# Performance work log

Hardware: AMD Instinct MI355X
Metric: run time of the kernel (lower is better)

The kernel has to match this reference:

```python
import jax, jax.numpy as jnp
import numpy as np

NEG_BIG = 1e9  # large-negative bias used by the original TF code


def setup_inputs() -> dict:
    key = jax.random.key(0)
    kq, kk, kv = jax.random.split(key, 3)
    B, H, W, C, CV = 8, 64, 64, 128, 128
    return {
        "query": jax.random.normal(kq, (B, H, W, C), dtype=jnp.float32),
        "key": jax.random.normal(kk, (B, H, W, C), dtype=jnp.float32),
        "value": jax.random.normal(kv, (B, H, W, CV), dtype=jnp.float32),
    }


def reference(query, key, value):
    B, Hh, Ww, C = query.shape
    CV = value.shape[-1]
    Nq = Hh * Ww                      # canvas_size_q (flattened spatial)
    Nk = key.shape[1] * key.shape[2]  # canvas_size
    q = query.reshape(B, Nq, C)
    k = key.reshape(B, Nk, C)
    v = value.reshape(B, Nk, CV)
    # dense QK^T scores over the flattened canvas: [B, Nq, Nk]
    dot = jnp.einsum('bqc,bkc->bqk', q, k) / jnp.sqrt(jnp.asarray(C, dtype=q.dtype))
    # causal mask: 1 where key position j <= query position i (allowed)
    allowed = jnp.tril(jnp.ones((Nq, Nk), dtype=q.dtype))
    # softmax with large-negative bias on disallowed positions, then re-mask
    probs = jax.nn.softmax(dot - NEG_BIG * (1.0 - allowed), axis=-1) * allowed
    mixed = jnp.einsum('bqk,bkc->bqc', probs, v)
    return mixed.reshape(B, Hh, Ww, CV)
```

## Files before the change

kernel.cpp:

```cpp
#include <hip/hip_runtime.h>
#include <hip/hip_bf16.h>

typedef __bf16 bf16_t;
typedef __attribute__((ext_vector_type(8))) __bf16 bf16x8;
typedef __attribute__((ext_vector_type(4))) __bf16 bf16x4;
typedef __attribute__((ext_vector_type(4))) float floatx4;

static constexpr int NSEQ = 4096;
static constexpr int DIM  = 128;
static constexpr int BATCH = 8;
static constexpr size_t NELEM = (size_t)BATCH * NSEQ * DIM;
static constexpr size_t WS_NEED = 2 * NELEM * sizeof(bf16_t);

static constexpr int NSLOT = 160;
static constexpr size_t WS_SPLITK =
    WS_NEED + (size_t)BATCH * NSLOT * (8192 + 64) * sizeof(float);

static constexpr float SCALE_LOG2E = 0.08838834764831845f * 1.4426950408889634f;

__device__ __forceinline__ int slot_base(int qt) {
  int g = qt >> 4, r = qt & 15;
  return qt + 8 * g * (g - 1) + r * g;
}

__device__ __forceinline__ void gld16(bf16_t* l, const bf16_t* g) {
  __builtin_amdgcn_global_load_lds(
      (const __attribute__((address_space(1))) unsigned int*)g,
      (__attribute__((address_space(3))) unsigned int*)l, 16, 0, 0);
}

__device__ __forceinline__ bf16x8 ld8_f32s(const float* p, float s) {
  float4 a = *(const float4*)p;
  float4 b = *(const float4*)(p + 4);
  bf16x8 r = {(__bf16)(a.x * s), (__bf16)(a.y * s), (__bf16)(a.z * s), (__bf16)(a.w * s),
              (__bf16)(b.x * s), (__bf16)(b.y * s), (__bf16)(b.z * s), (__bf16)(b.w * s)};
  return r;
}


__global__ __launch_bounds__(256)
void prep_kernel(const float* __restrict__ K, const float* __restrict__ V,
                 bf16_t* __restrict__ Kb, bf16_t* __restrict__ Vt) {
  __shared__ bf16_t ldsT[128 * 66];
  const int bid = blockIdx.x;
  if (bid < 1536) {
    const size_t n4 = NELEM / 4;
    for (size_t i = (size_t)bid * 256 + threadIdx.x; i < n4; i += (size_t)1536 * 256) {
      float4 k = ((const float4*)K)[i];
      bf16x4 kv = {(__bf16)k.x, (__bf16)k.y, (__bf16)k.z, (__bf16)k.w};
      ((bf16x4*)Kb)[i] = kv;
    }
  } else {
    const int id = bid - 1536;
    const int b  = id & 7;
    const int kt = id >> 3;
    const float* src = V + ((size_t)(b * NSEQ + kt * 64)) * DIM;
    #pragma unroll
    for (int it = 0; it < 8; ++it) {
      const int idx = it * 256 + (int)threadIdx.x;
      const int k = idx >> 5, c4 = idx & 31;
      float4 v = ((const float4*)src)[idx];
      ldsT[(c4 * 4 + 0) * 66 + k] = (__bf16)v.x;
      ldsT[(c4 * 4 + 1) * 66 + k] = (__bf16)v.y;
      ldsT[(c4 * 4 + 2) * 66 + k] = (__bf16)v.z;
      ldsT[(c4 * 4 + 3) * 66 + k] = (__bf16)v.w;
    }
    __syncthreads();
    #pragma unroll
    for (int it = 0; it < 4; ++it) {
      const int task = it * 256 + (int)threadIdx.x;
      const int d = task >> 3, kg = task & 7;
      bf16x8 o;
      #pragma unroll
      for (int j = 0; j < 8; ++j) o[j] = ldsT[d * 66 + kg * 8 + j];
      *(bf16x8*)(Vt + ((size_t)b * DIM + d) * NSEQ + kt * 64 + kg * 8) = o;
    }
  }
}


template <bool MASK>
__device__ __forceinline__ void tile16(
    const bf16_t* __restrict__ kbuf, const bf16_t* __restrict__ vbuf,
    const bf16x8 (&qf)[4], int l16, int quad, int wq16,
    floatx4 (&acc)[8], float& lsum) {
  #pragma unroll
  for (int h = 0; h < 2; ++h) {
    float pr[8];
    #pragma unroll
    for (int cc = 0; cc < 2; ++cc) {
      const int c4 = 2 * h + cc;
      floatx4 sv = {0.f, 0.f, 0.f, 0.f};
      const bf16_t* krow = kbuf + (c4 * 16 + l16) * DIM;
      #pragma unroll
      for (int d = 0; d < 4; ++d) {
        bf16x8 kf = *(const bf16x8*)(krow + (((4 * d + quad) ^ l16) * 8));
        sv = __builtin_amdgcn_mfma_f32_16x16x32_bf16(kf, qf[d], sv, 0, 0, 0);
      }
      #pragma unroll
      for (int r = 0; r < 4; ++r) {
        float v = sv[r];
        if constexpr (MASK) {
          const int key = 32 * h + 8 * quad + 4 * cc + r;
          v = (key <= wq16 + l16) ? v : -3.0e38f;
        }
        float p = __builtin_amdgcn_exp2f(v);
        lsum += p;
        pr[4 * cc + r] = p;
      }
    }
    bf16x8 pf;
    #pragma unroll
    for (int j = 0; j < 8; ++j) pf[j] = (__bf16)pr[j];
    __builtin_amdgcn_s_setprio(1);
    #pragma unroll
    for (int c = 0; c < 8; ++c) {
      const bf16_t* vrow = vbuf + (c * 16 + l16) * 64;
      bf16x8 vf = *(const bf16x8*)(vrow + (((quad + 4 * h) ^ (l16 & 7)) * 8));
      acc[c] = __builtin_amdgcn_mfma_f32_16x16x32_bf16(pf, vf, acc[c], 0, 0, 0);
    }
    __builtin_amdgcn_s_setprio(0);
  }
}


__global__ __launch_bounds__(256, 3)
void causal_attn_splitk(const float* __restrict__ Qf, const bf16_t* __restrict__ Kb,
                        const bf16_t* __restrict__ Vt, float* __restrict__ Out,
                        float* __restrict__ Pp, float* __restrict__ Ls) {
  __shared__ __align__(16) bf16_t Kds[2][64 * DIM];
  __shared__ __align__(16) bf16_t Vds[DIM * 64];

  const int b = (int)blockIdx.x & 7;
  const int s = (NSLOT - 1) - ((int)blockIdx.x >> 3);
  int qt = 63, cch = 0;
  {
    int acc0 = 0;
    #pragma unroll
    for (int g = 0; g < 4; ++g) {
      const int bandw = 16 * (g + 1);
      if (s < acc0 + bandw) {
        const int u = s - acc0;
        qt = g * 16 + u / (g + 1);
        cch = u % (g + 1);
        break;
      }
      acc0 += bandw;
    }
  }
  const int ntot = qt + 1;
  const int nch  = (qt >> 4) + 1;
  const int nt_c = (ntot - 1 - cch) / nch + 1;
  const int nmask = (cch + (nt_c - 1) * nch == qt) ? 1 : 0;
  const int nfull = nt_c - nmask;

  const int tid  = (int)threadIdx.x;
  const int wave = tid >> 6;
  const int lane = tid & 63;
  const int l16  = lane & 15;
  const int quad = lane >> 4;
  const int wq16 = wave * 16;

  bf16x8 qf[4];
  {
    const float* qrow =
        Qf + ((size_t)b * NSEQ + qt * 64 + wq16 + l16) * DIM + quad * 8;
    #pragma unroll
    for (int d = 0; d < 4; ++d) qf[d] = ld8_f32s(qrow + 32 * d, SCALE_LOG2E);
  }

  const bf16_t* kg = Kb + (size_t)b * NSEQ * DIM;
  const bf16_t* vg = Vt + ((size_t)b * DIM + 32 * wave) * NSEQ;
  int koff[4], voff[4], vsrc[4], vdst[4];
  #pragma unroll
  for (int i = 0; i < 4; ++i) {
    const int p    = 16 * wave + 4 * i + quad;
    const int srow = 32 * (wave >> 1) + 8 * i + 4 * (wave & 1) + quad;
    koff[i] = srow * DIM + ((l16 ^ (p & 15)) * 8);
    const int vrow = 8 * i + (lane >> 3);
    voff[i] = vrow * NSEQ + (((lane & 7) ^ (vrow & 7)) * 8);
    vsrc[i] = vrow * NSEQ + (lane & 7) * 8;
    vdst[i] = (32 * wave + vrow) * 64 + (((lane & 7) ^ (vrow & 7)) * 8);
  }

  floatx4 acc[8];
  #pragma unroll
  for (int c = 0; c < 8; ++c) acc[c] = (floatx4){0.f, 0.f, 0.f, 0.f};
  float lsum = 0.f;

  {
    const size_t kb0 = (size_t)cch * 64;
    bf16_t* kl = &Kds[0][wave * 2048];
    bf16_t* vl = &Vds[wave * 2048];
    #pragma unroll
    for (int i = 0; i < 4; ++i) {
      gld16(kl + i * 512, kg + kb0 * DIM + koff[i]);
      gld16(vl + i * 512, vg + kb0 + voff[i]);
    }
  }
  __syncthreads();

  bf16x8 vreg[4];
  int t = cch;
  for (int it = 0; it < nt_c; ++it, t += nch) {
    const int cur = it & 1;
    const bool more = (it + 1 < nt_c);
    const size_t kbn = (size_t)(t + nch) * 64;
    if (more) {
      bf16_t* kl = &Kds[cur ^ 1][wave * 2048];
      #pragma unroll
      for (int i = 0; i < 4; ++i) gld16(kl + i * 512, kg + kbn * DIM + koff[i]);
      #pragma unroll
      for (int i = 0; i < 4; ++i) vreg[i] = *(const bf16x8*)(vg + kbn + vsrc[i]);
    }
    __builtin_amdgcn_sched_barrier(0);
    if (it < nfull)
      tile16<false>(Kds[cur], Vds, qf, l16, quad, wq16, acc, lsum);
    else
      tile16<true>(Kds[cur], Vds, qf, l16, quad, wq16, acc, lsum);
    __builtin_amdgcn_sched_barrier(0);
    __builtin_amdgcn_s_barrier();
    if (more) {
      #pragma unroll
      for (int i = 0; i < 4; ++i) *(bf16x8*)(&Vds[vdst[i]]) = vreg[i];
      asm volatile("s_waitcnt lgkmcnt(0)" ::: "memory");
      __builtin_amdgcn_sched_barrier(0);
      __builtin_amdgcn_s_barrier();
    }
  }

  float lred = lsum;
  lred += __shfl_xor(lred, 16, 64);
  lred += __shfl_xor(lred, 32, 64);

  if (nch == 1) {
    float invl[4];
    #pragma unroll
    for (int r = 0; r < 4; ++r)
      invl[r] = 1.0f / __shfl(lred, quad * 4 + r, 64);
    float* orow =
        Out + ((size_t)b * NSEQ + qt * 64 + wq16 + quad * 4) * DIM + l16;
    #pragma unroll
    for (int c = 0; c < 8; ++c)
      #pragma unroll
      for (int r = 0; r < 4; ++r)
        orow[(size_t)r * DIM + c * 16] = acc[c][r] * invl[r];
  } else {
    const int slot = b * NSLOT + slot_base(qt) + cch;
    float* pb = Pp + (size_t)slot * 8192 +
                ((size_t)(wq16 + quad * 4)) * 128 + l16;
    #pragma unroll
    for (int c = 0; c < 8; ++c)
      #pragma unroll
      for (int r = 0; r < 4; ++r)
        pb[(size_t)r * 128 + c * 16] = acc[c][r];
    if (quad == 0)
      Ls[(size_t)slot * 64 + wq16 + l16] = lred;
  }
}


__global__ __launch_bounds__(256)
void combine_kernel(const float* __restrict__ Pp, const float* __restrict__ Ls,
                    float* __restrict__ Out) {
  const int e    = (int)blockIdx.x >> 1;
  const int half = (int)blockIdx.x & 1;
  const int b    = e & 7;
  const int qt   = 16 + (e >> 3);
  const int s0   = b * NSLOT + slot_base(qt);
  const int nch  = (qt >> 4) + 1;
  const int t = (int)threadIdx.x;
  #pragma unroll
  for (int j = 0; j < 4; ++j) {
    const int idx = j * 256 + t;
    const int q   = half * 32 + (idx >> 5);
    const int d4  = idx & 31;
    float4 v = {0.f, 0.f, 0.f, 0.f};
    float  l = 0.f;
    for (int ch = 0; ch < nch; ++ch) {
      const float* pc = Pp + (size_t)(s0 + ch) * 8192 + (size_t)q * 128 + d4 * 4;
      float4 a = *(const float4*)pc;
      v.x += a.x; v.y += a.y; v.z += a.z; v.w += a.w;
      l += Ls[(size_t)(s0 + ch) * 64 + q];
    }
    const float inv = 1.0f / l;
    float4 r = {v.x * inv, v.y * inv, v.z * inv, v.w * inv};
    *(float4*)(Out + ((size_t)b * NSEQ + qt * 64 + q) * DIM + d4 * 4) = r;
  }
}


template <bool MASK>
__device__ __forceinline__ void tile_compute(
    const bf16_t* __restrict__ kbuf, const bf16_t* __restrict__ vbuf,
    bf16_t* __restrict__ pl, const bf16x8 (&qf)[4],
    int l16, int quad, int wq, floatx4 (&acc)[8], float (&lsum)[4]) {
  floatx4 s[4];
  #pragma unroll
  for (int c4 = 0; c4 < 4; ++c4) s[c4] = (floatx4){0.f, 0.f, 0.f, 0.f};
  #pragma unroll
  for (int c4 = 0; c4 < 4; ++c4) {
    const bf16_t* krow = kbuf + (c4 * 16 + l16) * DIM;
    #pragma unroll
    for (int d = 0; d < 4; ++d) {
      bf16x8 kf = *(const bf16x8*)(krow + (((4 * d + quad) ^ l16) * 8));
      s[c4] = __builtin_amdgcn_mfma_f32_16x16x32_bf16(qf[d], kf, s[c4], 0, 0, 0);
    }
  }
  #pragma unroll
  for (int c4 = 0; c4 < 4; ++c4) {
    #pragma unroll
    for (int r = 0; r < 4; ++r) {
      float v = s[c4][r];
      if constexpr (MASK)
        v = (c4 * 16 + l16 <= wq + quad * 4 + r) ? v : -3.0e38f;
      float p = __builtin_amdgcn_exp2f(v);
      lsum[r] += p;
      pl[(quad * 4 + r) * 72 + c4 * 16 + l16] = (__bf16)p;
    }
  }
  asm volatile("s_waitcnt lgkmcnt(0)" ::: "memory");
  bf16x8 pfA = *(const bf16x8*)(pl + l16 * 72 + quad * 8);
  bf16x8 pfB = *(const bf16x8*)(pl + l16 * 72 + 32 + quad * 8);
  #pragma unroll
  for (int c = 0; c < 8; ++c) {
    const bf16_t* vrow = vbuf + (c * 16 + l16) * 64;
    bf16x8 vfA = *(const bf16x8*)(vrow + ((quad ^ (l16 & 7)) * 8));
    bf16x8 vfB = *(const bf16x8*)(vrow + (((quad + 4) ^ (l16 & 7)) * 8));
    acc[c] = __builtin_amdgcn_mfma_f32_16x16x32_bf16(pfA, vfA, acc[c], 0, 0, 0);
    acc[c] = __builtin_amdgcn_mfma_f32_16x16x32_bf16(pfB, vfB, acc[c], 0, 0, 0);
  }
}

__global__ __launch_bounds__(256)
void causal_attn_kernel(const float* __restrict__ Qf, const bf16_t* __restrict__ Kb,
                        const bf16_t* __restrict__ Vt, float* __restrict__ Out) {
  __shared__ __align__(16) bf16_t Kbuf[64 * DIM];
  __shared__ __align__(16) bf16_t Vbuf[DIM * 64];
  __shared__ __align__(16) bf16_t Pbuf[4][16 * 72];

  const int half = blockIdx.x >> 8;
  const int idx  = blockIdx.x & 255;
  const int b    = idx & 7;
  const int q32  = idx >> 3;
  const int qt64 = half ? q32 : 63 - q32;

  const int tid  = (int)threadIdx.x;
  const int wave = tid >> 6;
  const int lane = tid & 63;
  const int l16  = lane & 15;
  const int quad = lane >> 4;
  const int wq   = wave * 16;

  bf16x8 qf[4];
  {
    const float* qrow = Qf + ((size_t)b * NSEQ + qt64 * 64 + wq + l16) * DIM + quad * 8;
    #pragma unroll
    for (int d = 0; d < 4; ++d) qf[d] = ld8_f32s(qrow + 32 * d, SCALE_LOG2E);
  }

  const bf16_t* kg0 = Kb + ((size_t)b * NSEQ + 16 * wave) * DIM;
  const bf16_t* vg0 = Vt + ((size_t)b * DIM + 32 * wave) * NSEQ;
  int koff[4], voff[4];
  #pragma unroll
  for (int i = 0; i < 4; ++i) {
    const int krow = 4 * i + (lane >> 4);
    koff[i] = krow * DIM + (((lane & 15) ^ (krow & 15)) * 8);
    const int vrow = 8 * i + (lane >> 3);
    voff[i] = vrow * NSEQ + (((lane & 7) ^ ((lane >> 3) & 7)) * 8);
  }
  bf16_t* kl = Kbuf + 16 * wave * DIM;
  bf16_t* vl = Vbuf + 32 * wave * 64;
  bf16_t* pl = Pbuf[wave];

  floatx4 acc[8];
  #pragma unroll
  for (int c = 0; c < 8; ++c) acc[c] = (floatx4){0.f, 0.f, 0.f, 0.f};
  float lsum[4] = {0.f, 0.f, 0.f, 0.f};

  const int nk = qt64 + 1;
  for (int kt = 0; kt < nk - 1; ++kt) {
    const int kb = kt * 64;
    #pragma unroll
    for (int i = 0; i < 4; ++i) gld16(kl + i * 512, kg0 + (size_t)kb * DIM + koff[i]);
    #pragma unroll
    for (int i = 0; i < 4; ++i) gld16(vl + i * 512, vg0 + kb + voff[i]);
    __syncthreads();
    tile_compute<false>(Kbuf, Vbuf, pl, qf, l16, quad, wq, acc, lsum);
    __syncthreads();
  }
  {
    const int kb = (nk - 1) * 64;
    #pragma unroll
    for (int i = 0; i < 4; ++i) gld16(kl + i * 512, kg0 + (size_t)kb * DIM + koff[i]);
    #pragma unroll
    for (int i = 0; i < 4; ++i) gld16(vl + i * 512, vg0 + kb + voff[i]);
    __syncthreads();
    tile_compute<true>(Kbuf, Vbuf, pl, qf, l16, quad, wq, acc, lsum);
  }

  float inv_l[4];
  #pragma unroll
  for (int r = 0; r < 4; ++r) {
    float s = lsum[r];
    #pragma unroll
    for (int off = 1; off < 16; off <<= 1) s += __shfl_xor(s, off, 64);
    inv_l[r] = 1.0f / s;
  }
  float* orow = Out + ((size_t)b * NSEQ + qt64 * 64 + wq + quad * 4) * DIM + l16;
  #pragma unroll
  for (int c = 0; c < 8; ++c) {
    #pragma unroll
    for (int r = 0; r < 4; ++r)
      orow[(size_t)r * DIM + c * 16] = acc[c][r] * inv_l[r];
  }
}


__global__ __launch_bounds__(256)
void causal_attn_fb(const float* __restrict__ Qf, const float* __restrict__ Kf,
                    const float* __restrict__ Vf, float* __restrict__ Out) {
  __shared__ bf16_t p_lds[4][16 * 72];
  const int bid = blockIdx.x, t = bid >> 3, b = bid & 7;
  const int tid = (int)threadIdx.x, wave = tid >> 6, lane = tid & 63;
  const int l16 = lane & 15, quad = lane >> 4;
  const int qtile = (wave < 2) ? t : (127 - t);
  const int q_base = qtile * 32 + (wave & 1) * 16;

  bf16x8 qf[4];
  const float* qrow = Qf + ((size_t)b * NSEQ + q_base + l16) * DIM + quad * 8;
  #pragma unroll
  for (int d = 0; d < 4; ++d) qf[d] = ld8_f32s(qrow + 32 * d, SCALE_LOG2E);

  floatx4 acc[8];
  #pragma unroll
  for (int c = 0; c < 8; ++c) acc[c] = (floatx4){0.f, 0.f, 0.f, 0.f};
  float lsum[4] = {0.f, 0.f, 0.f, 0.f};
  bf16_t* pl = p_lds[wave];
  const int ntiles = (q_base + 16 + 63) >> 6;

  for (int kt = 0; kt < ntiles; ++kt) {
    const int kb = kt * 64;
    floatx4 s[4];
    #pragma unroll
    for (int c4 = 0; c4 < 4; ++c4) s[c4] = (floatx4){0.f, 0.f, 0.f, 0.f};
    const float* kbase = Kf + ((size_t)b * NSEQ + kb + l16) * DIM + quad * 8;
    #pragma unroll
    for (int c4 = 0; c4 < 4; ++c4) {
      #pragma unroll
      for (int d = 0; d < 4; ++d) {
        bf16x8 kf = ld8_f32s(kbase + (size_t)c4 * 16 * DIM + 32 * d, 1.0f);
        s[c4] = __builtin_amdgcn_mfma_f32_16x16x32_bf16(qf[d], kf, s[c4], 0, 0, 0);
      }
    }
    #pragma unroll
    for (int c4 = 0; c4 < 4; ++c4) {
      #pragma unroll
      for (int r = 0; r < 4; ++r) {
        float v = s[c4][r];
        const int qi = q_base + quad * 4 + r;
        v = (kb + c4 * 16 + l16 <= qi) ? v : -3.0e38f;
        float p = __builtin_amdgcn_exp2f(v);
        lsum[r] += p;
        pl[(quad * 4 + r) * 72 + c4 * 16 + l16] = (__bf16)p;
      }
    }
    asm volatile("s_waitcnt lgkmcnt(0)" ::: "memory");
    bf16x8 pfA = *(const bf16x8*)(pl + l16 * 72 + quad * 8);
    bf16x8 pfB = *(const bf16x8*)(pl + l16 * 72 + 32 + quad * 8);
    const float* vb = Vf + ((size_t)b * NSEQ + kb) * DIM;
    #pragma unroll
    for (int c = 0; c < 8; ++c) {
      bf16x8 vfA, vfB;
      #pragma unroll
      for (int j = 0; j < 8; ++j) {
        vfA[j] = (__bf16)vb[(size_t)(quad * 8 + j) * DIM + c * 16 + l16];
        vfB[j] = (__bf16)vb[(size_t)(32 + quad * 8 + j) * DIM + c * 16 + l16];
      }
      acc[c] = __builtin_amdgcn_mfma_f32_16x16x32_bf16(pfA, vfA, acc[c], 0, 0, 0);
      acc[c] = __builtin_amdgcn_mfma_f32_16x16x32_bf16(pfB, vfB, acc[c], 0, 0, 0);
    }
  }
  float inv_l[4];
  #pragma unroll
  for (int r = 0; r < 4; ++r) {
    float s = lsum[r];
    #pragma unroll
    for (int off = 1; off < 16; off <<= 1) s += __shfl_xor(s, off, 64);
    inv_l[r] = 1.0f / s;
  }
  float* orow = Out + ((size_t)b * NSEQ + q_base + quad * 4) * DIM + l16;
  #pragma unroll
  for (int c = 0; c < 8; ++c) {
    #pragma unroll
    for (int r = 0; r < 4; ++r)
      orow[(size_t)r * DIM + c * 16] = acc[c][r] * inv_l[r];
  }
}

extern "C" void kernel_launch(void* const* d_in, const int* in_sizes, int n_in,
                              void* d_out, int out_size, void* d_ws, size_t ws_size,
                              hipStream_t stream) {
  const float* Q = (const float*)d_in[0];
  const float* K = (const float*)d_in[1];
  const float* V = (const float*)d_in[2];
  float* Out = (float*)d_out;
  (void)in_sizes; (void)n_in; (void)out_size;

  dim3 block(256);
  if (ws_size >= WS_SPLITK) {
    bf16_t* Kb = (bf16_t*)d_ws;
    bf16_t* Vt = Kb + NELEM;
    float*  Pp = (float*)((char*)d_ws + WS_NEED);
    float*  Ls = Pp + (size_t)BATCH * NSLOT * 8192;
    prep_kernel<<<dim3(2048), block, 0, stream>>>(K, V, Kb, Vt);
    causal_attn_splitk<<<dim3(BATCH * NSLOT), block, 0, stream>>>(Q, Kb, Vt, Out, Pp, Ls);
    combine_kernel<<<dim3(BATCH * 48 * 2), block, 0, stream>>>(Pp, Ls, Out);
  } else if (ws_size >= WS_NEED) {
    bf16_t* Kb = (bf16_t*)d_ws;
    bf16_t* Vt = Kb + NELEM;
    prep_kernel<<<dim3(2048), block, 0, stream>>>(K, V, Kb, Vt);
    causal_attn_kernel<<<dim3(512), block, 0, stream>>>(Q, Kb, Vt, Out);
  } else {
    causal_attn_fb<<<dim3(512), block, 0, stream>>>(Q, K, V, Out);
  }
}
```

Before: 153.9 us.

## Fuse split-K combine into attention kernel via last-block atomic counter

Drops the separate combine kernel. The last split-K block to finish for a (batch, query-tile) now does the reduction, detected with an atomic counter held in the workspace and zeroed by prep_kernel. The K fp32-to-bf16 conversion in prep is also widened to 8 elements per thread. This removes one kernel launch and lets the reduction read partials that are likely still in cache. In exchange it adds threadfences, an atomic per block and a serialized tail reduction inside the attention blocks.

Result: slower. 358.4 us (+132.9%).

```diff
diff --git a/kernel.cpp b/kernel.cpp
--- a/kernel.cpp
+++ b/kernel.cpp
@@ -40,15 +40,22 @@
 
 __global__ __launch_bounds__(256)
 void prep_kernel(const float* __restrict__ K, const float* __restrict__ V,
-                 bf16_t* __restrict__ Kb, bf16_t* __restrict__ Vt) {
+                 bf16_t* __restrict__ Kb, bf16_t* __restrict__ Vt,
+                 float* __restrict__ Pp) {
   __shared__ bf16_t ldsT[128 * 66];
   const int bid = blockIdx.x;
+  if (Pp != nullptr && bid == 0) {
+    ((int*)Pp)[threadIdx.x] = 0;
+    ((int*)Pp)[256 + threadIdx.x] = 0;
+  }
   if (bid < 1536) {
-    const size_t n4 = NELEM / 4;
-    for (size_t i = (size_t)bid * 256 + threadIdx.x; i < n4; i += (size_t)1536 * 256) {
-      float4 k = ((const float4*)K)[i];
-      bf16x4 kv = {(__bf16)k.x, (__bf16)k.y, (__bf16)k.z, (__bf16)k.w};
-      ((bf16x4*)Kb)[i] = kv;
+    const size_t n8 = NELEM / 8;
+    for (size_t i = (size_t)bid * 256 + threadIdx.x; i < n8; i += (size_t)1536 * 256) {
+      float4 a = ((const float4*)K)[2 * i];
+      float4 c = ((const float4*)K)[2 * i + 1];
+      bf16x8 kv = {(__bf16)a.x, (__bf16)a.y, (__bf16)a.z, (__bf16)a.w,
+                   (__bf16)c.x, (__bf16)c.y, (__bf16)c.z, (__bf16)c.w};
+      ((bf16x8*)Kb)[i] = kv;
     }
   } else {
     const int id = bid - 1536;
@@ -130,6 +137,7 @@
                         float* __restrict__ Pp, float* __restrict__ Ls) {
   __shared__ __align__(16) bf16_t Kds[2][64 * DIM];
   __shared__ __align__(16) bf16_t Vds[DIM * 64];
+  __shared__ int is_last;
 
   const int b = (int)blockIdx.x & 7;
   const int s = (NSLOT - 1) - ((int)blockIdx.x >> 3);
@@ -246,7 +254,8 @@
       for (int r = 0; r < 4; ++r)
         orow[(size_t)r * DIM + c * 16] = acc[c][r] * invl[r];
   } else {
-    const int slot = b * NSLOT + slot_base(qt) + cch;
+    const int s0   = b * NSLOT + slot_base(qt);
+    const int slot = s0 + cch;
     float* pb = Pp + (size_t)slot * 8192 +
                 ((size_t)(wq16 + quad * 4)) * 128 + l16;
     #pragma unroll
@@ -256,36 +265,32 @@
         pb[(size_t)r * 128 + c * 16] = acc[c][r];
     if (quad == 0)
       Ls[(size_t)slot * 64 + wq16 + l16] = lred;
-  }
-}
-
-
-__global__ __launch_bounds__(256)
-void combine_kernel(const float* __restrict__ Pp, const float* __restrict__ Ls,
-                    float* __restrict__ Out) {
-  const int e    = (int)blockIdx.x >> 1;
-  const int half = (int)blockIdx.x & 1;
-  const int b    = e & 7;
-  const int qt   = 16 + (e >> 3);
-  const int s0   = b * NSLOT + slot_base(qt);
-  const int nch  = (qt >> 4) + 1;
-  const int t = (int)threadIdx.x;
-  #pragma unroll
-  for (int j = 0; j < 4; ++j) {
-    const int idx = j * 256 + t;
-    const int q   = half * 32 + (idx >> 5);
-    const int d4  = idx & 31;
-    float4 v = {0.f, 0.f, 0.f, 0.f};
-    float  l = 0.f;
-    for (int ch = 0; ch < nch; ++ch) {
-      const float* pc = Pp + (size_t)(s0 + ch) * 8192 + (size_t)q * 128 + d4 * 4;
-      float4 a = *(const float4*)pc;
-      v.x += a.x; v.y += a.y; v.z += a.z; v.w += a.w;
-      l += Ls[(size_t)(s0 + ch) * 64 + q];
-    }
-    const float inv = 1.0f / l;
-    float4 r = {v.x * inv, v.y * inv, v.z * inv, v.w * inv};
-    *(float4*)(Out + ((size_t)b * NSEQ + qt * 64 + q) * DIM + d4 * 4) = r;
+
+    __threadfence();
+    __syncthreads();
+    if (tid == 0)
+      is_last = (atomicAdd(&((int*)Pp)[b * 64 + qt], 1) == nch - 1);
+    __syncthreads();
+    if (is_last) {
+      __threadfence();
+      #pragma unroll
+      for (int j = 0; j < 8; ++j) {
+        const int idx = j * 256 + tid;
+        const int q   = idx >> 5;
+        const int d4  = idx & 31;
+        float4 v = {0.f, 0.f, 0.f, 0.f};
+        float  l = 0.f;
+        for (int ch = 0; ch < nch; ++ch) {
+          const float* pc = Pp + (size_t)(s0 + ch) * 8192 + (size_t)q * 128 + d4 * 4;
+          float4 a = *(const float4*)pc;
+          v.x += a.x; v.y += a.y; v.z += a.z; v.w += a.w;
+          l += Ls[(size_t)(s0 + ch) * 64 + q];
+        }
+        const float inv = 1.0f / l;
+        float4 r = {v.x * inv, v.y * inv, v.z * inv, v.w * inv};
+        *(float4*)(Out + ((size_t)b * NSEQ + qt * 64 + q) * DIM + d4 * 4) = r;
+      }
+    }
   }
 }
 
@@ -513,13 +518,12 @@
     bf16_t* Vt = Kb + NELEM;
     float*  Pp = (float*)((char*)d_ws + WS_NEED);
     float*  Ls = Pp + (size_t)BATCH * NSLOT * 8192;
-    prep_kernel<<<dim3(2048), block, 0, stream>>>(K, V, Kb, Vt);
+    prep_kernel<<<dim3(2048), block, 0, stream>>>(K, V, Kb, Vt, Pp);
     causal_attn_splitk<<<dim3(BATCH * NSLOT), block, 0, stream>>>(Q, Kb, Vt, Out, Pp, Ls);
-    combine_kernel<<<dim3(BATCH * 48 * 2), block, 0, stream>>>(Pp, Ls, Out);
   } else if (ws_size >= WS_NEED) {
     bf16_t* Kb = (bf16_t*)d_ws;
     bf16_t* Vt = Kb + NELEM;
-    prep_kernel<<<dim3(2048), block, 0, stream>>>(K, V, Kb, Vt);
+    prep_kernel<<<dim3(2048), block, 0, stream>>>(K, V, Kb, Vt, nullptr);
     causal_attn_kernel<<<dim3(512), block, 0, stream>>>(Q, Kb, Vt, Out);
   } else {
     causal_attn_fb<<<dim3(512), block, 0, stream>>>(Q, K, V, Out);
```
